# Performance work log

Hardware: AMD Instinct MI355X
Metric: run time of the kernel (lower is better)

Reference implementation:

```python
import jax, jax.numpy as jnp
import numpy as np

B, P, E = 64, 196, 2048      # batch, num_pixels (14*14), encoder_size
H, EMB, V = 512, 512, 10000  # hidden_size, embed_size, vocab_size
T_CAP = 50                   # hard-coded pred/alpha buffer length
T_MAX = T_CAP - 1            # max(decode_lengths) = max(lengths) - 1 = 49


def setup_inputs() -> dict:
    key = jax.random.key(0)
    ks = jax.random.split(key, 20)

    def lin(k, out_f, in_f):
        kw, kb = jax.random.split(k)
        s = 1.0 / np.sqrt(in_f)
        return (jax.random.uniform(kw, (out_f, in_f), jnp.float32, -s, s),
                jax.random.uniform(kb, (out_f,), jnp.float32, -s, s))

    features = jax.random.normal(ks[0], (B, P, E), jnp.float32)
    captions = jax.random.randint(ks[1], (B, T_CAP), 0, V)
    # sorted descending, first length forced to 50 so max(decode_lengths)=49
    lengths = jnp.sort(jax.random.randint(ks[2], (B,), 2, T_CAP + 1))[::-1]
    lengths = lengths.at[0].set(T_CAP)

    Wx_w, Wx_b = lin(ks[3], E, E)          # attention Wx: encoder->encoder
    Wh_w, Wh_b = lin(ks[4], E, H)          # attention Wh: hidden->encoder
    V_w, V_b = lin(ks[5], 1, E)            # attention V: encoder->1
    init_h_w, init_h_b = lin(ks[6], H, E)  # init_h
    f_beta_w, f_beta_b = lin(ks[7], E, H)  # f_beta gate
    embed_w = jax.random.normal(ks[8], (V, EMB), jnp.float32)
    gru_w_ih, gru_b_ih = lin(ks[9], 3 * H, E + EMB)
    gru_w_hh, gru_b_hh = lin(ks[10], 3 * H, H)
    fc1_w, fc1_b = lin(ks[11], V, H)

    return dict(features=features, captions=captions, lengths=lengths,
                Wx_w=Wx_w, Wx_b=Wx_b, Wh_w=Wh_w, Wh_b=Wh_b, V_w=V_w, V_b=V_b,
                init_h_w=init_h_w, init_h_b=init_h_b,
                f_beta_w=f_beta_w, f_beta_b=f_beta_b, embed_w=embed_w,
                gru_w_ih=gru_w_ih, gru_b_ih=gru_b_ih,
                gru_w_hh=gru_w_hh, gru_b_hh=gru_b_hh,
                fc1_w=fc1_w, fc1_b=fc1_b)


def reference(features, captions, lengths, Wx_w, Wx_b, Wh_w, Wh_b, V_w, V_b,
              init_h_w, init_h_b, f_beta_w, f_beta_b, embed_w,
              gru_w_ih, gru_b_ih, gru_w_hh, gru_b_hh, fc1_w, fc1_b):
    b, p, e = features.shape
    vsz = fc1_w.shape[0]
    dec = lengths - 1                                  # decode_lengths
    # init hidden state from mean-pooled features
    h0 = jnp.mean(features, axis=1) @ init_h_w.T + init_h_b      # [B,H]
    # Wx(features) is time-invariant: precompute once
    x_wx = jnp.einsum('bpe,fe->bpf', features, Wx_w) + Wx_b      # [B,P,E]
    emb = embed_w[captions]                                      # [B,50,EMB]
    emb_t = jnp.transpose(emb[:, :T_MAX], (1, 0, 2))             # [T,B,EMB]

    def step(h, xs):
        t, e_t = xs
        active = (dec >= t)                            # rows still decoding
        # Bahdanau attention
        h_wh = h @ Wh_w.T + Wh_b                       # [B,E]
        lam = jnp.einsum('bpe,oe->bpo',
                         jnp.tanh(x_wx + h_wh[:, None, :]), V_w) + V_b
        alpha = jax.nn.softmax(lam, axis=1)            # [B,P,1]
        z = jnp.sum(alpha * features, axis=1)          # [B,E]
        # sigmoid gate
        gate = jax.nn.sigmoid(h @ f_beta_w.T + f_beta_b)
        inp = jnp.concatenate([gate * z, e_t], axis=1)  # [B,E+EMB]
        # GRUCell (torch gate order r,z,n)
        gi = inp @ gru_w_ih.T + gru_b_ih
        gh = h @ gru_w_hh.T + gru_b_hh
        i_r, i_z, i_n = jnp.split(gi, 3, axis=-1)
        h_r, h_z, h_n = jnp.split(gh, 3, axis=-1)
        r = jax.nn.sigmoid(i_r + h_r)
        zg = jax.nn.sigmoid(i_z + h_z)
        n = jnp.tanh(i_n + r * h_n)
        h_new = (1.0 - zg) * n + zg * h
        pred = h_new @ fc1_w.T + fc1_b                 # dropout in eval = id
        m = active[:, None]
        h_out = jnp.where(m, h_new, h)                 # freeze finished rows
        return h_out, (jnp.where(m, pred, 0.0),
                       jnp.where(m, alpha[..., 0], 0.0))

    _, (preds_t, alphas_t) = jax.lax.scan(
        step, h0, (jnp.arange(T_MAX), emb_t))
    preds = jnp.zeros((b, T_CAP, vsz), features.dtype)
    preds = preds.at[:, :T_MAX].set(jnp.transpose(preds_t, (1, 0, 2)))
    alphas = jnp.zeros((b, T_CAP, p), features.dtype)
    alphas = alphas.at[:, :T_MAX].set(jnp.transpose(alphas_t, (1, 0, 2)))
    return preds, alphas, dec
```

## Files before the change

### kernel.cpp

```cpp
#include <hip/hip_runtime.h>
#include <cstddef>

#define B_    64
#define P_    196
#define E_    2048
#define H_    512
#define EMB_  512
#define V_    10000
#define TCAP_ 50
#define TMAX_ 49
#define KI_   2560
#define G3_   1536

typedef __attribute__((ext_vector_type(8))) short short8;
typedef __attribute__((ext_vector_type(4))) float floatx4;
typedef unsigned int u32;
typedef const __attribute__((address_space(1))) u32* gptr_t;
typedef __attribute__((address_space(3))) u32* lptr_t;

__device__ __forceinline__ unsigned short f2bf_rne(float f) {
    unsigned int x = __float_as_uint(f);
    unsigned int r = (x + 0x7fffu + ((x >> 16) & 1u)) >> 16;
    return (unsigned short)r;
}
__device__ __forceinline__ float bf2f(unsigned int u16) {
    return __uint_as_float(u16 << 16);
}
__device__ __forceinline__ float fast_tanh(float x) {
    float a = fabsf(x);
    float e = __expf(2.0f * a);
    float r = 1.0f - 2.0f / (e + 1.0f);
    return (x < 0.0f) ? -r : r;
}
__device__ __forceinline__ float fast_sig(float x) {
    return 1.0f / (1.0f + __expf(-x));
}

__global__ void init_out_kernel(float* __restrict__ preds, float* __restrict__ alphas,
                                float* __restrict__ dec, const int* __restrict__ lens)
{
    int i = blockIdx.x * 256 + threadIdx.x;
    if (i < B_ * V_) {
        int b = i / V_, v = i - b * V_;
        preds[((size_t)b * TCAP_ + TMAX_) * V_ + v] = 0.f;
    }
    if (i < B_ * P_) {
        int b = i / P_, p = i - b * P_;
        alphas[((size_t)b * TCAP_ + TMAX_) * P_ + p] = 0.f;
    }
    if (i < B_) dec[i] = (float)(lens[i] - 1);
}

__global__ void f2bf_kernel(const float* __restrict__ src, unsigned short* __restrict__ dst, int n8)
{
    int i = blockIdx.x * 256 + threadIdx.x;
    if (i >= n8) return;
    float4 a = ((const float4*)src)[2 * i];
    float4 b = ((const float4*)src)[2 * i + 1];
    uint4 o;
    o.x = (unsigned)f2bf_rne(a.x) | ((unsigned)f2bf_rne(a.y) << 16);
    o.y = (unsigned)f2bf_rne(a.z) | ((unsigned)f2bf_rne(a.w) << 16);
    o.z = (unsigned)f2bf_rne(b.x) | ((unsigned)f2bf_rne(b.y) << 16);
    o.w = (unsigned)f2bf_rne(b.z) | ((unsigned)f2bf_rne(b.w) << 16);
    ((uint4*)dst)[i] = o;
}

__global__ void mean_kernel(const float* __restrict__ f, unsigned short* __restrict__ out)
{
    int i = blockIdx.x * 256 + threadIdx.x;
    int b = i >> 11, e = i & 2047;
    const float* p = f + (size_t)b * P_ * E_ + e;
    float s = 0.f;
    #pragma unroll 4
    for (int k = 0; k < P_; ++k) s += p[(size_t)k * E_];
    out[i] = f2bf_rne(s * (1.0f / (float)P_));
}

__global__ void __launch_bounds__(256)
mfma_xwx_kernel(const unsigned short* __restrict__ A,
                const unsigned short* __restrict__ W,
                const float* __restrict__ bias,
                unsigned short* __restrict__ C)
{
    __shared__ unsigned short As[128 * 64];
    __shared__ unsigned short Bs[128 * 64];
    int wv = threadIdx.x >> 6, lane = threadIdx.x & 63;
    int mr = lane & 15, quad = lane >> 4;
    int m0 = blockIdx.y * 128;
    int n0 = blockIdx.x * 128;
    int wm = (wv & 1) * 64, wn = (wv >> 1) * 64;
    int srow = wv * 32;
    int lrow = lane >> 3;
    int lcol = (lane & 7) * 8;
    floatx4 acc[4][4] = {};
    for (int k0 = 0; k0 < E_; k0 += 64) {
        __syncthreads();
        #pragma unroll
        for (int i = 0; i < 4; ++i) {
            int r = srow + i * 8;
            __builtin_amdgcn_global_load_lds(
                (gptr_t)(A + (size_t)(m0 + r + lrow) * E_ + k0 + lcol),
                (lptr_t)(As + r * 64), 16, 0, 0);
            __builtin_amdgcn_global_load_lds(
                (gptr_t)(W + (size_t)(n0 + r + lrow) * E_ + k0 + lcol),
                (lptr_t)(Bs + r * 64), 16, 0, 0);
        }
        __syncthreads();
        #pragma unroll
        for (int kk = 0; kk < 64; kk += 32) {
            short8 af[4], bf[4];
            #pragma unroll
            for (int i = 0; i < 4; ++i)
                af[i] = *(const short8*)(As + (wm + i * 16 + mr) * 64 + kk + quad * 8);
            #pragma unroll
            for (int j = 0; j < 4; ++j)
                bf[j] = *(const short8*)(Bs + (wn + j * 16 + mr) * 64 + kk + quad * 8);
            #pragma unroll
            for (int i = 0; i < 4; ++i)
                #pragma unroll
                for (int j = 0; j < 4; ++j)
                    acc[i][j] = __builtin_amdgcn_mfma_f32_16x16x32_bf16(af[i], bf[j], acc[i][j], 0, 0, 0);
        }
    }
    #pragma unroll
    for (int j = 0; j < 4; ++j) {
        int col = n0 + wn + j * 16 + mr;
        float bs = bias[col];
        #pragma unroll
        for (int i = 0; i < 4; ++i) {
            int row = m0 + wm + i * 16 + quad * 4;
            #pragma unroll
            for (int ii = 0; ii < 4; ++ii)
                C[(size_t)(row + ii) * E_ + col] = f2bf_rne(acc[i][j][ii] + bs);
        }
    }
}

__global__ void __launch_bounds__(256)
fc1tile_kernel(const unsigned short* __restrict__ Hall,
               const unsigned short* __restrict__ W,
               const float* __restrict__ bias,
               float* __restrict__ preds, const int* __restrict__ lens)
{
    __shared__ unsigned short As[128 * 64];
    __shared__ unsigned short Bs[128 * 64];
    int wv = threadIdx.x >> 6, lane = threadIdx.x & 63;
    int mr = lane & 15, quad = lane >> 4;
    int m0 = blockIdx.y * 128;
    int n0 = blockIdx.x * 128;
    int wm = (wv & 1) * 64, wn = (wv >> 1) * 64;
    int srow = wv * 32;
    int lrow = lane >> 3;
    int lcol = (lane & 7) * 8;
    floatx4 acc[4][4] = {};
    for (int k0 = 0; k0 < H_; k0 += 64) {
        __syncthreads();
        #pragma unroll
        for (int i = 0; i < 4; ++i) {
            int r = srow + i * 8;
            __builtin_amdgcn_global_load_lds(
                (gptr_t)(Hall + (size_t)(m0 + r + lrow) * H_ + k0 + lcol),
                (lptr_t)(As + r * 64), 16, 0, 0);
            __builtin_amdgcn_global_load_lds(
                (gptr_t)(W + (size_t)(n0 + r + lrow) * H_ + k0 + lcol),
                (lptr_t)(Bs + r * 64), 16, 0, 0);
        }
        __syncthreads();
        #pragma unroll
        for (int kk = 0; kk < 64; kk += 32) {
            short8 af[4], bf[4];
            #pragma unroll
            for (int i = 0; i < 4; ++i)
                af[i] = *(const short8*)(As + (wm + i * 16 + mr) * 64 + kk + quad * 8);
            #pragma unroll
            for (int j = 0; j < 4; ++j)
                bf[j] = *(const short8*)(Bs + (wn + j * 16 + mr) * 64 + kk + quad * 8);
            #pragma unroll
            for (int i = 0; i < 4; ++i)
                #pragma unroll
                for (int j = 0; j < 4; ++j)
                    acc[i][j] = __builtin_amdgcn_mfma_f32_16x16x32_bf16(af[i], bf[j], acc[i][j], 0, 0, 0);
        }
    }
    #pragma unroll
    for (int j = 0; j < 4; ++j) {
        int col = n0 + wn + j * 16 + mr;
        float bs = bias[min(col, V_ - 1)];
        #pragma unroll
        for (int i = 0; i < 4; ++i) {
            int row = m0 + wm + i * 16 + quad * 4;
            #pragma unroll
            for (int ii = 0; ii < 4; ++ii) {
                int r = row + ii;
                if (r < TMAX_ * B_ && col < V_) {
                    int t = r >> 6, b = r & 63;
                    float v = (lens[b] > t) ? (acc[i][j][ii] + bs) : 0.f;
                    preds[((size_t)b * TCAP_ + t) * V_ + col] = v;
                }
            }
        }
    }
}

template<int KC>
__global__ void __launch_bounds__(256)
mfma_gemm64(const unsigned short* __restrict__ A, int ld,
            const unsigned short* __restrict__ W,
            const float* __restrict__ bias,
            float* __restrict__ C, unsigned short* __restrict__ Cbf, int ldc)
{
    int wv = threadIdx.x >> 6, lane = threadIdx.x & 63;
    int mr = lane & 15, quad = lane >> 4;
    int m0 = wv * 16;
    int n0 = blockIdx.x * 16;
    const unsigned short* pa = A + (size_t)(m0 + mr) * ld + quad * 8;
    const unsigned short* pb = W + (size_t)(n0 + mr) * ld + quad * 8;
    floatx4 acc = {0.f, 0.f, 0.f, 0.f};
    #pragma unroll 16
    for (int k0 = 0; k0 < KC; k0 += 32) {
        short8 a = *(const short8*)(const void*)(pa + k0);
        short8 b = *(const short8*)(const void*)(pb + k0);
        acc = __builtin_amdgcn_mfma_f32_16x16x32_bf16(a, b, acc, 0, 0, 0);
    }
    int col = n0 + mr;
    float bs = bias ? bias[col] : 0.f;
    #pragma unroll
    for (int i = 0; i < 4; ++i) {
        int row = m0 + quad * 4 + i;
        float v = acc[i] + bs;
        C[(size_t)row * ldc + col] = v;
        if (Cbf) Cbf[(size_t)row * ldc + col] = f2bf_rne(v);
    }
}

__global__ void __launch_bounds__(256)
mfma_h3(const unsigned short* __restrict__ hbf,
        const unsigned short* __restrict__ whbf, const float* __restrict__ Wh_b,
        const unsigned short* __restrict__ fbbf, const float* __restrict__ fb_b,
        const unsigned short* __restrict__ ghhbf, const float* __restrict__ ghh_b,
        float* __restrict__ hwh, float* __restrict__ hf, float* __restrict__ gh)
{
    int bt = blockIdx.x;
    const unsigned short* W; const float* bias; float* C; int n0; int ldc;
    if (bt < 128)      { W = whbf;  bias = Wh_b;  C = hwh; n0 = bt * 16;         ldc = E_; }
    else if (bt < 256) { W = fbbf;  bias = fb_b;  C = hf;  n0 = (bt - 128) * 16; ldc = E_; }
    else               { W = ghhbf; bias = ghh_b; C = gh;  n0 = (bt - 256) * 16; ldc = G3_; }
    int wv = threadIdx.x >> 6, lane = threadIdx.x & 63;
    int mr = lane & 15, quad = lane >> 4;
    int m0 = wv * 16;
    const unsigned short* pa = hbf + (size_t)(m0 + mr) * H_ + quad * 8;
    const unsigned short* pb = W + (size_t)(n0 + mr) * H_ + quad * 8;
    floatx4 acc0 = {0.f, 0.f, 0.f, 0.f};
    floatx4 acc1 = {0.f, 0.f, 0.f, 0.f};
    #pragma unroll
    for (int k0 = 0; k0 < 256; k0 += 32) {
        short8 a0 = *(const short8*)(const void*)(pa + k0);
        short8 b0 = *(const short8*)(const void*)(pb + k0);
        acc0 = __builtin_amdgcn_mfma_f32_16x16x32_bf16(a0, b0, acc0, 0, 0, 0);
        short8 a1 = *(const short8*)(const void*)(pa + k0 + 256);
        short8 b1 = *(const short8*)(const void*)(pb + k0 + 256);
        acc1 = __builtin_amdgcn_mfma_f32_16x16x32_bf16(a1, b1, acc1, 0, 0, 0);
    }
    floatx4 acc = acc0 + acc1;
    int col = n0 + mr;
    float bs = bias[col];
    #pragma unroll
    for (int i = 0; i < 4; ++i) {
        int row = m0 + quad * 4 + i;
        C[(size_t)row * ldc + col] = acc[i] + bs;
    }
}

__global__ void __launch_bounds__(256)
lam_kernel(const unsigned short* __restrict__ xwx, const float* __restrict__ hwh,
           const float* __restrict__ Vw, const float* __restrict__ Vb,
           float* __restrict__ lam)
{
    __shared__ float sh[E_];
    __shared__ float sv[E_];
    int b = blockIdx.y;
    int p0 = blockIdx.x * 16;
    int tid = threadIdx.x;
    {
        const float4* hs = (const float4*)(hwh + (size_t)b * E_);
        const float4* vs = (const float4*)Vw;
        ((float4*)sh)[tid]       = hs[tid];
        ((float4*)sh)[tid + 256] = hs[tid + 256];
        ((float4*)sv)[tid]       = vs[tid];
        ((float4*)sv)[tid + 256] = vs[tid + 256];
    }
    __syncthreads();
    int wv = tid >> 6, lane = tid & 63;
    #pragma unroll
    for (int r = 0; r < 4; ++r) {
        int p = p0 + wv * 4 + r;
        if (p < P_) {
            const unsigned short* px = xwx + ((size_t)b * P_ + p) * E_;
            float acc = 0.f;
            #pragma unroll
            for (int it = 0; it < 4; ++it) {
                int e = it * 512 + lane * 8;
                uint4 u = *(const uint4*)(const void*)(px + e);
                float4 h0 = *(const float4*)(sh + e);
                float4 h1 = *(const float4*)(sh + e + 4);
                float4 v0 = *(const float4*)(sv + e);
                float4 v1 = *(const float4*)(sv + e + 4);
                acc = fmaf(fast_tanh(bf2f(u.x & 0xffffu) + h0.x), v0.x, acc);
                acc = fmaf(fast_tanh(bf2f(u.x >> 16)     + h0.y), v0.y, acc);
                acc = fmaf(fast_tanh(bf2f(u.y & 0xffffu) + h0.z), v0.z, acc);
                acc = fmaf(fast_tanh(bf2f(u.y >> 16)     + h0.w), v0.w, acc);
                acc = fmaf(fast_tanh(bf2f(u.z & 0xffffu) + h1.x), v1.x, acc);
                acc = fmaf(fast_tanh(bf2f(u.z >> 16)     + h1.y), v1.y, acc);
                acc = fmaf(fast_tanh(bf2f(u.w & 0xffffu) + h1.z), v1.z, acc);
                acc = fmaf(fast_tanh(bf2f(u.w >> 16)     + h1.w), v1.w, acc);
            }
            #pragma unroll
            for (int off = 32; off > 0; off >>= 1) acc += __shfl_down(acc, off);
            if (lane == 0) lam[b * P_ + p] = acc + Vb[0];
        }
    }
}

__global__ void __launch_bounds__(256)
attn_z_kernel(const unsigned short* __restrict__ fbf, const float* __restrict__ lam,
              const float* __restrict__ hf, const float* __restrict__ embed_w,
              const int* __restrict__ captions, const int* __restrict__ lens,
              unsigned short* __restrict__ inpbf, float* __restrict__ alphas, int t)
{
    int b = blockIdx.y;
    int tile = blockIdx.x;
    int tid = threadIdx.x;
    if (tile == 4) {
        int cap = captions[b * TCAP_ + t];
        const float* e = embed_w + (size_t)cap * EMB_;
        int c = tid * 2;
        float2 v = *(const float2*)(e + c);
        *(unsigned int*)(inpbf + (size_t)b * KI_ + E_ + c) =
            (unsigned)f2bf_rne(v.x) | ((unsigned)f2bf_rne(v.y) << 16);
        return;
    }
    __shared__ float sa[256];
    __shared__ float sr[256];
    __shared__ float psum[4][64][8];
    float x = (tid < P_) ? lam[b * P_ + tid] : -1e30f;
    sr[tid] = x;
    __syncthreads();
    for (int s = 128; s > 0; s >>= 1) {
        if (tid < s) sr[tid] = fmaxf(sr[tid], sr[tid + s]);
        __syncthreads();
    }
    float mx = sr[0];
    __syncthreads();
    float ex = (tid < P_) ? __expf(x - mx) : 0.f;
    sa[tid] = ex;
    sr[tid] = ex;
    __syncthreads();
    for (int s = 128; s > 0; s >>= 1) {
        if (tid < s) sr[tid] += sr[tid + s];
        __syncthreads();
    }
    float inv = 1.0f / sr[0];
    if (tile == 0 && tid < P_) {
        alphas[(size_t)b * TCAP_ * P_ + (size_t)t * P_ + tid] = (lens[b] > t) ? ex * inv : 0.f;
    }
    int wv = tid >> 6, lane = tid & 63;
    int e0 = tile * 512;
    const unsigned short* fp = fbf + ((size_t)b * P_ + wv * 49) * E_ + e0 + lane * 8;
    float acc[8] = {0.f,0.f,0.f,0.f,0.f,0.f,0.f,0.f};
    #pragma unroll 7
    for (int i = 0; i < 49; ++i) {
        uint4 u = *(const uint4*)(const void*)(fp + (size_t)i * E_);
        float ap = sa[wv * 49 + i];
        acc[0] = fmaf(ap, bf2f(u.x & 0xffffu), acc[0]);
        acc[1] = fmaf(ap, bf2f(u.x >> 16),     acc[1]);
        acc[2] = fmaf(ap, bf2f(u.y & 0xffffu), acc[2]);
        acc[3] = fmaf(ap, bf2f(u.y >> 16),     acc[3]);
        acc[4] = fmaf(ap, bf2f(u.z & 0xffffu), acc[4]);
        acc[5] = fmaf(ap, bf2f(u.z >> 16),     acc[5]);
        acc[6] = fmaf(ap, bf2f(u.w & 0xffffu), acc[6]);
        acc[7] = fmaf(ap, bf2f(u.w >> 16),     acc[7]);
    }
    #pragma unroll
    for (int k = 0; k < 8; ++k) psum[wv][lane][k] = acc[k];
    __syncthreads();
    int c0 = tid * 2;
    int lc = c0 >> 3, kc = c0 & 7;
    float2 s = {0.f, 0.f};
    #pragma unroll
    for (int w2 = 0; w2 < 4; ++w2) {
        float2 v = *(const float2*)&psum[w2][lc][kc];
        s.x += v.x; s.y += v.y;
    }
    s.x *= inv; s.y *= inv;
    float2 gv = *(const float2*)(hf + (size_t)b * E_ + e0 + c0);
    float g0 = fast_sig(gv.x), g1 = fast_sig(gv.y);
    *(unsigned int*)(inpbf + (size_t)b * KI_ + e0 + c0) =
        (unsigned)f2bf_rne(g0 * s.x) | ((unsigned)f2bf_rne(g1 * s.y) << 16);
}

__global__ void __launch_bounds__(256)
gigru_kernel(const unsigned short* __restrict__ inpbf,
             const unsigned short* __restrict__ wihbf,
             const float* __restrict__ b_ih,
             const float* __restrict__ gh,
             const int* __restrict__ lens,
             float* __restrict__ h, unsigned short* __restrict__ hbf,
             unsigned short* __restrict__ Hall, int t)
{
    __shared__ float red[4][3][16][17];
    int wv = threadIdx.x >> 6, lane = threadIdx.x & 63;
    int mr = lane & 15, quad = lane >> 4;
    int j0 = blockIdx.x * 16;
    int m0 = blockIdx.y * 16;
    int koff = wv * 640;
    const unsigned short* pa = inpbf + (size_t)(m0 + mr) * KI_ + koff + quad * 8;
    const unsigned short* pb0 = wihbf + (size_t)(j0 + mr) * KI_ + koff + quad * 8;
    const unsigned short* pb1 = pb0 + (size_t)512 * KI_;
    const unsigned short* pb2 = pb0 + (size_t)1024 * KI_;
    floatx4 ar = {0.f,0.f,0.f,0.f}, az = {0.f,0.f,0.f,0.f}, an = {0.f,0.f,0.f,0.f};
    #pragma unroll 4
    for (int k0 = 0; k0 < 640; k0 += 32) {
        short8 a = *(const short8*)(const void*)(pa + k0);
        short8 br = *(const short8*)(const void*)(pb0 + k0);
        short8 bz = *(const short8*)(const void*)(pb1 + k0);
        short8 bn = *(const short8*)(const void*)(pb2 + k0);
        ar = __builtin_amdgcn_mfma_f32_16x16x32_bf16(a, br, ar, 0, 0, 0);
        az = __builtin_amdgcn_mfma_f32_16x16x32_bf16(a, bz, az, 0, 0, 0);
        an = __builtin_amdgcn_mfma_f32_16x16x32_bf16(a, bn, an, 0, 0, 0);
    }
    #pragma unroll
    for (int i = 0; i < 4; ++i) {
        red[wv][0][quad * 4 + i][mr] = ar[i];
        red[wv][1][quad * 4 + i][mr] = az[i];
        red[wv][2][quad * 4 + i][mr] = an[i];
    }
    __syncthreads();
    int row = threadIdx.x >> 4, col = threadIdx.x & 15;
    int b = m0 + row, j = j0 + col;
    float ir = red[0][0][row][col] + red[1][0][row][col] + red[2][0][row][col] + red[3][0][row][col] + b_ih[j];
    float iz = red[0][1][row][col] + red[1][1][row][col] + red[2][1][row][col] + red[3][1][row][col] + b_ih[512 + j];
    float in_= red[0][2][row][col] + red[1][2][row][col] + red[2][2][row][col] + red[3][2][row][col] + b_ih[1024 + j];
    float hr = gh[(size_t)b * G3_ + j];
    float hz = gh[(size_t)b * G3_ + 512 + j];
    float hn = gh[(size_t)b * G3_ + 1024 + j];
    float r  = fast_sig(ir + hr);
    float zg = fast_sig(iz + hz);
    float n  = fast_tanh(in_ + r * hn);
    float hp = h[(size_t)b * H_ + j];
    float hv = (1.f - zg) * n + zg * hp;
    float ho = (lens[b] > t) ? hv : hp;
    h[(size_t)b * H_ + j] = ho;
    unsigned short hob = f2bf_rne(ho);
    hbf[(size_t)b * H_ + j] = hob;
    Hall[((size_t)t * B_ + b) * H_ + j] = hob;
}

extern "C" void kernel_launch(void* const* d_in, const int* in_sizes, int n_in,
                              void* d_out, int out_size, void* d_ws, size_t ws_size,
                              hipStream_t stream)
{
    const float* features  = (const float*)d_in[0];
    const int*   captions  = (const int*)d_in[1];
    const int*   lengths   = (const int*)d_in[2];
    const float* Wx_w      = (const float*)d_in[3];
    const float* Wx_b      = (const float*)d_in[4];
    const float* Wh_w      = (const float*)d_in[5];
    const float* Wh_b      = (const float*)d_in[6];
    const float* V_w       = (const float*)d_in[7];
    const float* V_b       = (const float*)d_in[8];
    const float* init_h_w  = (const float*)d_in[9];
    const float* init_h_b  = (const float*)d_in[10];
    const float* f_beta_w  = (const float*)d_in[11];
    const float* f_beta_b  = (const float*)d_in[12];
    const float* embed_w   = (const float*)d_in[13];
    const float* gru_w_ih  = (const float*)d_in[14];
    const float* gru_b_ih  = (const float*)d_in[15];
    const float* gru_w_hh  = (const float*)d_in[16];
    const float* gru_b_hh  = (const float*)d_in[17];
    const float* fc1_w     = (const float*)d_in[18];
    const float* fc1_b     = (const float*)d_in[19];

    float* preds  = (float*)d_out;
    float* alphas = preds + (size_t)B_ * TCAP_ * V_;
    float* dec    = alphas + (size_t)B_ * TCAP_ * P_;

    char* w = (char*)d_ws;
    unsigned short* fbf     = (unsigned short*)w; w += (size_t)12544 * 2048 * 2;
    unsigned short* xwx     = (unsigned short*)w; w += (size_t)12544 * 2048 * 2;
    unsigned short* wxbf    = (unsigned short*)w; w += (size_t)2048 * 2048 * 2;
    unsigned short* whbf    = (unsigned short*)w; w += (size_t)2048 * 512 * 2;
    unsigned short* fbbf    = (unsigned short*)w; w += (size_t)2048 * 512 * 2;
    unsigned short* ghhbf   = (unsigned short*)w; w += (size_t)1536 * 512 * 2;
    unsigned short* wihbf   = (unsigned short*)w; w += (size_t)1536 * 2560 * 2;
    unsigned short* fc1bf   = (unsigned short*)w; w += (size_t)10112 * 512 * 2;
    unsigned short* ihwbf   = (unsigned short*)w; w += (size_t)512 * 2048 * 2;
    unsigned short* fmeanbf = (unsigned short*)w; w += (size_t)64 * 2048 * 2;
    unsigned short* hbf     = (unsigned short*)w; w += (size_t)64 * 512 * 2;
    unsigned short* inpbf   = (unsigned short*)w; w += (size_t)64 * KI_ * 2;
    unsigned short* Hall    = (unsigned short*)w; w += (size_t)3200 * 512 * 2;
    float* h   = (float*)w; w += (size_t)64 * 512 * 4;
    float* hwh = (float*)w; w += (size_t)64 * 2048 * 4;
    float* hf  = (float*)w; w += (size_t)64 * 2048 * 4;
    float* gh  = (float*)w; w += (size_t)64 * 1536 * 4;
    float* lam = (float*)w; w += (size_t)64 * 196 * 4;

    init_out_kernel<<<2500, 256, 0, stream>>>(preds, alphas, dec, lengths);

    f2bf_kernel<<<12544, 256, 0, stream>>>(features, fbf, 12544 * 2048 / 8);
    f2bf_kernel<<<2048, 256, 0, stream>>>(Wx_w, wxbf, 2048 * 2048 / 8);
    f2bf_kernel<<<512, 256, 0, stream>>>(Wh_w, whbf, 2048 * 512 / 8);
    f2bf_kernel<<<512, 256, 0, stream>>>(f_beta_w, fbbf, 2048 * 512 / 8);
    f2bf_kernel<<<384, 256, 0, stream>>>(gru_w_hh, ghhbf, 1536 * 512 / 8);
    f2bf_kernel<<<1920, 256, 0, stream>>>(gru_w_ih, wihbf, 1536 * 2560 / 8);
    f2bf_kernel<<<2500, 256, 0, stream>>>(fc1_w, fc1bf, 10000 * 512 / 8);
    f2bf_kernel<<<512, 256, 0, stream>>>(init_h_w, ihwbf, 512 * 2048 / 8);

    mean_kernel<<<512, 256, 0, stream>>>(features, fmeanbf);
    mfma_gemm64<2048><<<32, 256, 0, stream>>>(fmeanbf, 2048, ihwbf, init_h_b, h, hbf, 512);
    mfma_xwx_kernel<<<dim3(16, 98), 256, 0, stream>>>(fbf, wxbf, Wx_b, xwx);

    for (int t = 0; t < TMAX_; ++t) {
        mfma_h3<<<352, 256, 0, stream>>>(hbf, whbf, Wh_b, fbbf, f_beta_b, ghhbf, gru_b_hh,
                                         hwh, hf, gh);
        lam_kernel<<<dim3(13, 64), 256, 0, stream>>>(xwx, hwh, V_w, V_b, lam);
        attn_z_kernel<<<dim3(5, 64), 256, 0, stream>>>(fbf, lam, hf, embed_w, captions,
                                                       lengths, inpbf, alphas, t);
        gigru_kernel<<<dim3(32, 4), 256, 0, stream>>>(inpbf, wihbf, gru_b_ih, gh,
                                                      lengths, h, hbf, Hall, t);
    }
    fc1tile_kernel<<<dim3(79, 25), 256, 0, stream>>>(Hall, fc1bf, fc1_b, preds, lengths);
}
```

Before: 3.326 ms.

## Fuse recurrent decode loop into persistent kernel with atomic grid barriers

Replaces the 49x4 per-timestep kernel launches with one persistent 512-block kernel that runs every decode step, separating the phases with an atomic-counter grid barrier. The attention-context phase is also re-split from 5 tiles per batch to 8 column chunks of 256, and softmax reductions now use wave shuffles. This is meant to remove launch overhead and inter-kernel gaps on a latency-bound recurrence. The cost is that it depends on all 512 blocks being co-resident (256 CUs at 2 blocks each), and the spin barrier adds atomic traffic; the barrier also uses no cooperative launch, so a deadlock is possible if occupancy assumptions fail.

```diff
diff --git a/kernel.cpp b/kernel.cpp
--- a/kernel.cpp
+++ b/kernel.cpp
@@ -11,6 +11,7 @@
 #define TMAX_ 49
 #define KI_   2560
 #define G3_   1536
+#define NBLK_ 512
 
 typedef __attribute__((ext_vector_type(8))) short short8;
 typedef __attribute__((ext_vector_type(4))) float floatx4;
@@ -36,10 +37,25 @@
     return 1.0f / (1.0f + __expf(-x));
 }
 
+__device__ __forceinline__ void gbar(unsigned int* cnt, unsigned int target)
+{
+    __syncthreads();
+    if (threadIdx.x == 0) {
+        __threadfence();
+        atomicAdd(cnt, 1u);
+        while (__hip_atomic_load(cnt, __ATOMIC_RELAXED, __HIP_MEMORY_SCOPE_AGENT) < target)
+            __builtin_amdgcn_s_sleep(2);
+        __threadfence();
+    }
+    __syncthreads();
+}
+
 __global__ void init_out_kernel(float* __restrict__ preds, float* __restrict__ alphas,
-                                float* __restrict__ dec, const int* __restrict__ lens)
+                                float* __restrict__ dec, const int* __restrict__ lens,
+                                unsigned int* __restrict__ barcnt)
 {
     int i = blockIdx.x * 256 + threadIdx.x;
+    if (i == 0) *barcnt = 0u;
     if (i < B_ * V_) {
         int b = i / V_, v = i - b * V_;
         preds[((size_t)b * TCAP_ + TMAX_) * V_ + v] = 0.f;
@@ -233,226 +249,205 @@
     }
 }
 
-__global__ void __launch_bounds__(256)
-mfma_h3(const unsigned short* __restrict__ hbf,
-        const unsigned short* __restrict__ whbf, const float* __restrict__ Wh_b,
-        const unsigned short* __restrict__ fbbf, const float* __restrict__ fb_b,
-        const unsigned short* __restrict__ ghhbf, const float* __restrict__ ghh_b,
-        float* __restrict__ hwh, float* __restrict__ hf, float* __restrict__ gh)
-{
-    int bt = blockIdx.x;
-    const unsigned short* W; const float* bias; float* C; int n0; int ldc;
-    if (bt < 128)      { W = whbf;  bias = Wh_b;  C = hwh; n0 = bt * 16;         ldc = E_; }
-    else if (bt < 256) { W = fbbf;  bias = fb_b;  C = hf;  n0 = (bt - 128) * 16; ldc = E_; }
-    else               { W = ghhbf; bias = ghh_b; C = gh;  n0 = (bt - 256) * 16; ldc = G3_; }
-    int wv = threadIdx.x >> 6, lane = threadIdx.x & 63;
-    int mr = lane & 15, quad = lane >> 4;
-    int m0 = wv * 16;
-    const unsigned short* pa = hbf + (size_t)(m0 + mr) * H_ + quad * 8;
-    const unsigned short* pb = W + (size_t)(n0 + mr) * H_ + quad * 8;
-    floatx4 acc0 = {0.f, 0.f, 0.f, 0.f};
-    floatx4 acc1 = {0.f, 0.f, 0.f, 0.f};
-    #pragma unroll
-    for (int k0 = 0; k0 < 256; k0 += 32) {
-        short8 a0 = *(const short8*)(const void*)(pa + k0);
-        short8 b0 = *(const short8*)(const void*)(pb + k0);
-        acc0 = __builtin_amdgcn_mfma_f32_16x16x32_bf16(a0, b0, acc0, 0, 0, 0);
-        short8 a1 = *(const short8*)(const void*)(pa + k0 + 256);
-        short8 b1 = *(const short8*)(const void*)(pb + k0 + 256);
-        acc1 = __builtin_amdgcn_mfma_f32_16x16x32_bf16(a1, b1, acc1, 0, 0, 0);
-    }
-    floatx4 acc = acc0 + acc1;
-    int col = n0 + mr;
-    float bs = bias[col];
-    #pragma unroll
-    for (int i = 0; i < 4; ++i) {
-        int row = m0 + quad * 4 + i;
-        C[(size_t)row * ldc + col] = acc[i] + bs;
-    }
-}
-
-__global__ void __launch_bounds__(256)
-lam_kernel(const unsigned short* __restrict__ xwx, const float* __restrict__ hwh,
-           const float* __restrict__ Vw, const float* __restrict__ Vb,
-           float* __restrict__ lam)
-{
-    __shared__ float sh[E_];
-    __shared__ float sv[E_];
-    int b = blockIdx.y;
-    int p0 = blockIdx.x * 16;
-    int tid = threadIdx.x;
-    {
-        const float4* hs = (const float4*)(hwh + (size_t)b * E_);
-        const float4* vs = (const float4*)Vw;
-        ((float4*)sh)[tid]       = hs[tid];
-        ((float4*)sh)[tid + 256] = hs[tid + 256];
-        ((float4*)sv)[tid]       = vs[tid];
-        ((float4*)sv)[tid + 256] = vs[tid + 256];
-    }
-    __syncthreads();
-    int wv = tid >> 6, lane = tid & 63;
-    #pragma unroll
-    for (int r = 0; r < 4; ++r) {
-        int p = p0 + wv * 4 + r;
-        if (p < P_) {
-            const unsigned short* px = xwx + ((size_t)b * P_ + p) * E_;
-            float acc = 0.f;
-            #pragma unroll
-            for (int it = 0; it < 4; ++it) {
-                int e = it * 512 + lane * 8;
-                uint4 u = *(const uint4*)(const void*)(px + e);
-                float4 h0 = *(const float4*)(sh + e);
-                float4 h1 = *(const float4*)(sh + e + 4);
-                float4 v0 = *(const float4*)(sv + e);
-                float4 v1 = *(const float4*)(sv + e + 4);
-                acc = fmaf(fast_tanh(bf2f(u.x & 0xffffu) + h0.x), v0.x, acc);
-                acc = fmaf(fast_tanh(bf2f(u.x >> 16)     + h0.y), v0.y, acc);
-                acc = fmaf(fast_tanh(bf2f(u.y & 0xffffu) + h0.z), v0.z, acc);
-                acc = fmaf(fast_tanh(bf2f(u.y >> 16)     + h0.w), v0.w, acc);
-                acc = fmaf(fast_tanh(bf2f(u.z & 0xffffu) + h1.x), v1.x, acc);
-                acc = fmaf(fast_tanh(bf2f(u.z >> 16)     + h1.y), v1.y, acc);
-                acc = fmaf(fast_tanh(bf2f(u.w & 0xffffu) + h1.z), v1.z, acc);
-                acc = fmaf(fast_tanh(bf2f(u.w >> 16)     + h1.w), v1.w, acc);
-            }
-            #pragma unroll
-            for (int off = 32; off > 0; off >>= 1) acc += __shfl_down(acc, off);
-            if (lane == 0) lam[b * P_ + p] = acc + Vb[0];
-        }
-    }
-}
-
-__global__ void __launch_bounds__(256)
-attn_z_kernel(const unsigned short* __restrict__ fbf, const float* __restrict__ lam,
-              const float* __restrict__ hf, const float* __restrict__ embed_w,
-              const int* __restrict__ captions, const int* __restrict__ lens,
-              unsigned short* __restrict__ inpbf, float* __restrict__ alphas, int t)
-{
-    int b = blockIdx.y;
-    int tile = blockIdx.x;
-    int tid = threadIdx.x;
-    if (tile == 4) {
-        int cap = captions[b * TCAP_ + t];
-        const float* e = embed_w + (size_t)cap * EMB_;
-        int c = tid * 2;
-        float2 v = *(const float2*)(e + c);
-        *(unsigned int*)(inpbf + (size_t)b * KI_ + E_ + c) =
-            (unsigned)f2bf_rne(v.x) | ((unsigned)f2bf_rne(v.y) << 16);
-        return;
-    }
-    __shared__ float sa[256];
-    __shared__ float sr[256];
-    __shared__ float psum[4][64][8];
-    float x = (tid < P_) ? lam[b * P_ + tid] : -1e30f;
-    sr[tid] = x;
-    __syncthreads();
-    for (int s = 128; s > 0; s >>= 1) {
-        if (tid < s) sr[tid] = fmaxf(sr[tid], sr[tid + s]);
-        __syncthreads();
-    }
-    float mx = sr[0];
-    __syncthreads();
-    float ex = (tid < P_) ? __expf(x - mx) : 0.f;
-    sa[tid] = ex;
-    sr[tid] = ex;
-    __syncthreads();
-    for (int s = 128; s > 0; s >>= 1) {
-        if (tid < s) sr[tid] += sr[tid + s];
-        __syncthreads();
-    }
-    float inv = 1.0f / sr[0];
-    if (tile == 0 && tid < P_) {
-        alphas[(size_t)b * TCAP_ * P_ + (size_t)t * P_ + tid] = (lens[b] > t) ? ex * inv : 0.f;
-    }
-    int wv = tid >> 6, lane = tid & 63;
-    int e0 = tile * 512;
-    const unsigned short* fp = fbf + ((size_t)b * P_ + wv * 49) * E_ + e0 + lane * 8;
-    float acc[8] = {0.f,0.f,0.f,0.f,0.f,0.f,0.f,0.f};
-    #pragma unroll 7
-    for (int i = 0; i < 49; ++i) {
-        uint4 u = *(const uint4*)(const void*)(fp + (size_t)i * E_);
-        float ap = sa[wv * 49 + i];
-        acc[0] = fmaf(ap, bf2f(u.x & 0xffffu), acc[0]);
-        acc[1] = fmaf(ap, bf2f(u.x >> 16),     acc[1]);
-        acc[2] = fmaf(ap, bf2f(u.y & 0xffffu), acc[2]);
-        acc[3] = fmaf(ap, bf2f(u.y >> 16),     acc[3]);
-        acc[4] = fmaf(ap, bf2f(u.z & 0xffffu), acc[4]);
-        acc[5] = fmaf(ap, bf2f(u.z >> 16),     acc[5]);
-        acc[6] = fmaf(ap, bf2f(u.w & 0xffffu), acc[6]);
-        acc[7] = fmaf(ap, bf2f(u.w >> 16),     acc[7]);
-    }
-    #pragma unroll
-    for (int k = 0; k < 8; ++k) psum[wv][lane][k] = acc[k];
-    __syncthreads();
-    int c0 = tid * 2;
-    int lc = c0 >> 3, kc = c0 & 7;
-    float2 s = {0.f, 0.f};
-    #pragma unroll
-    for (int w2 = 0; w2 < 4; ++w2) {
-        float2 v = *(const float2*)&psum[w2][lc][kc];
-        s.x += v.x; s.y += v.y;
-    }
-    s.x *= inv; s.y *= inv;
-    float2 gv = *(const float2*)(hf + (size_t)b * E_ + e0 + c0);
-    float g0 = fast_sig(gv.x), g1 = fast_sig(gv.y);
-    *(unsigned int*)(inpbf + (size_t)b * KI_ + e0 + c0) =
-        (unsigned)f2bf_rne(g0 * s.x) | ((unsigned)f2bf_rne(g1 * s.y) << 16);
-}
-
-__global__ void __launch_bounds__(256)
-gigru_kernel(const unsigned short* __restrict__ inpbf,
-             const unsigned short* __restrict__ wihbf,
-             const float* __restrict__ b_ih,
-             const float* __restrict__ gh,
-             const int* __restrict__ lens,
-             float* __restrict__ h, unsigned short* __restrict__ hbf,
-             unsigned short* __restrict__ Hall, int t)
-{
-    __shared__ float red[4][3][16][17];
-    int wv = threadIdx.x >> 6, lane = threadIdx.x & 63;
-    int mr = lane & 15, quad = lane >> 4;
-    int j0 = blockIdx.x * 16;
-    int m0 = blockIdx.y * 16;
-    int koff = wv * 640;
-    const unsigned short* pa = inpbf + (size_t)(m0 + mr) * KI_ + koff + quad * 8;
-    const unsigned short* pb0 = wihbf + (size_t)(j0 + mr) * KI_ + koff + quad * 8;
-    const unsigned short* pb1 = pb0 + (size_t)512 * KI_;
-    const unsigned short* pb2 = pb0 + (size_t)1024 * KI_;
-    floatx4 ar = {0.f,0.f,0.f,0.f}, az = {0.f,0.f,0.f,0.f}, an = {0.f,0.f,0.f,0.f};
-    #pragma unroll 4
-    for (int k0 = 0; k0 < 640; k0 += 32) {
-        short8 a = *(const short8*)(const void*)(pa + k0);
-        short8 br = *(const short8*)(const void*)(pb0 + k0);
-        short8 bz = *(const short8*)(const void*)(pb1 + k0);
-        short8 bn = *(const short8*)(const void*)(pb2 + k0);
-        ar = __builtin_amdgcn_mfma_f32_16x16x32_bf16(a, br, ar, 0, 0, 0);
-        az = __builtin_amdgcn_mfma_f32_16x16x32_bf16(a, bz, az, 0, 0, 0);
-        an = __builtin_amdgcn_mfma_f32_16x16x32_bf16(a, bn, an, 0, 0, 0);
-    }
-    #pragma unroll
-    for (int i = 0; i < 4; ++i) {
-        red[wv][0][quad * 4 + i][mr] = ar[i];
-        red[wv][1][quad * 4 + i][mr] = az[i];
-        red[wv][2][quad * 4 + i][mr] = an[i];
-    }
-    __syncthreads();
-    int row = threadIdx.x >> 4, col = threadIdx.x & 15;
-    int b = m0 + row, j = j0 + col;
-    float ir = red[0][0][row][col] + red[1][0][row][col] + red[2][0][row][col] + red[3][0][row][col] + b_ih[j];
-    float iz = red[0][1][row][col] + red[1][1][row][col] + red[2][1][row][col] + red[3][1][row][col] + b_ih[512 + j];
-    float in_= red[0][2][row][col] + red[1][2][row][col] + red[2][2][row][col] + red[3][2][row][col] + b_ih[1024 + j];
-    float hr = gh[(size_t)b * G3_ + j];
-    float hz = gh[(size_t)b * G3_ + 512 + j];
-    float hn = gh[(size_t)b * G3_ + 1024 + j];
-    float r  = fast_sig(ir + hr);
-    float zg = fast_sig(iz + hz);
-    float n  = fast_tanh(in_ + r * hn);
-    float hp = h[(size_t)b * H_ + j];
-    float hv = (1.f - zg) * n + zg * hp;
-    float ho = (lens[b] > t) ? hv : hp;
-    h[(size_t)b * H_ + j] = ho;
-    unsigned short hob = f2bf_rne(ho);
-    hbf[(size_t)b * H_ + j] = hob;
-    Hall[((size_t)t * B_ + b) * H_ + j] = hob;
+__global__ void __launch_bounds__(256, 2)
+loop_kernel(unsigned short* __restrict__ hbf,
+            const unsigned short* __restrict__ whbf, const float* __restrict__ Wh_b,
+            const unsigned short* __restrict__ fbbf, const float* __restrict__ fb_b,
+            const unsigned short* __restrict__ ghhbf, const float* __restrict__ ghh_b,
+            float* __restrict__ hwh, float* __restrict__ hf, float* __restrict__ gh,
+            const unsigned short* __restrict__ xwx,
+            const float* __restrict__ Vw, const float* __restrict__ Vb,
+            float* __restrict__ lam,
+            const unsigned short* __restrict__ fbf,
+            const float* __restrict__ embed_w,
+            const int* __restrict__ captions, const int* __restrict__ lens,
+            unsigned short* __restrict__ inpbf,
+            float* __restrict__ alphas,
+            const unsigned short* __restrict__ wihbf, const float* __restrict__ b_ih,
+            float* __restrict__ h, unsigned short* __restrict__ Hall,
+            unsigned int* __restrict__ barcnt)
+{
+    __shared__ float smem[4096];
+    const int bid = blockIdx.x;
+    const int tid = threadIdx.x;
+    const int wv = tid >> 6, lane = tid & 63;
+    const int mr = lane & 15, quad = lane >> 4;
+    unsigned int ep = 0;
+
+    for (int t = 0; t < TMAX_; ++t) {
+        if (bid < 352) {
+            const unsigned short* W; const float* bias; float* C; int n0; int ldc;
+            if (bid < 128)      { W = whbf;  bias = Wh_b;  C = hwh; n0 = bid * 16;         ldc = E_; }
+            else if (bid < 256) { W = fbbf;  bias = fb_b;  C = hf;  n0 = (bid - 128) * 16; ldc = E_; }
+            else                { W = ghhbf; bias = ghh_b; C = gh;  n0 = (bid - 256) * 16; ldc = G3_; }
+            int m0 = wv * 16;
+            const unsigned short* pa = hbf + (size_t)(m0 + mr) * H_ + quad * 8;
+            const unsigned short* pb = W + (size_t)(n0 + mr) * H_ + quad * 8;
+            floatx4 acc0 = {0.f, 0.f, 0.f, 0.f};
+            floatx4 acc1 = {0.f, 0.f, 0.f, 0.f};
+            #pragma unroll
+            for (int k0 = 0; k0 < 256; k0 += 32) {
+                short8 a0 = *(const short8*)(const void*)(pa + k0);
+                short8 b0 = *(const short8*)(const void*)(pb + k0);
+                acc0 = __builtin_amdgcn_mfma_f32_16x16x32_bf16(a0, b0, acc0, 0, 0, 0);
+                short8 a1 = *(const short8*)(const void*)(pa + k0 + 256);
+                short8 b1 = *(const short8*)(const void*)(pb + k0 + 256);
+                acc1 = __builtin_amdgcn_mfma_f32_16x16x32_bf16(a1, b1, acc1, 0, 0, 0);
+            }
+            floatx4 acc = acc0 + acc1;
+            int col = n0 + mr;
+            float bs = bias[col];
+            #pragma unroll
+            for (int i = 0; i < 4; ++i)
+                C[(size_t)(m0 + quad * 4 + i) * ldc + col] = acc[i] + bs;
+        }
+        gbar(barcnt, (++ep) * (unsigned)NBLK_);
+
+        {
+            int b = bid >> 3, q = bid & 7;
+            float* sh = smem;
+            float* sv = smem + 2048;
+            const float4* hs = (const float4*)(hwh + (size_t)b * E_);
+            const float4* vs = (const float4*)Vw;
+            ((float4*)sh)[tid]       = hs[tid];
+            ((float4*)sh)[tid + 256] = hs[tid + 256];
+            ((float4*)sv)[tid]       = vs[tid];
+            ((float4*)sv)[tid + 256] = vs[tid + 256];
+            __syncthreads();
+            float vb0 = Vb[0];
+            #pragma unroll
+            for (int i = 0; i < 7; ++i) {
+                int pl = wv + i * 4;
+                int p = q * 25 + pl;
+                if (pl < 25 && p < P_) {
+                    const unsigned short* px = xwx + ((size_t)b * P_ + p) * E_;
+                    float acc = 0.f;
+                    #pragma unroll
+                    for (int it = 0; it < 4; ++it) {
+                        int e = it * 512 + lane * 8;
+                        uint4 u = *(const uint4*)(const void*)(px + e);
+                        float4 h0 = *(const float4*)(sh + e);
+                        float4 h1 = *(const float4*)(sh + e + 4);
+                        float4 v0 = *(const float4*)(sv + e);
+                        float4 v1 = *(const float4*)(sv + e + 4);
+                        acc = fmaf(fast_tanh(bf2f(u.x & 0xffffu) + h0.x), v0.x, acc);
+                        acc = fmaf(fast_tanh(bf2f(u.x >> 16)     + h0.y), v0.y, acc);
+                        acc = fmaf(fast_tanh(bf2f(u.y & 0xffffu) + h0.z), v0.z, acc);
+                        acc = fmaf(fast_tanh(bf2f(u.y >> 16)     + h0.w), v0.w, acc);
+                        acc = fmaf(fast_tanh(bf2f(u.z & 0xffffu) + h1.x), v1.x, acc);
+                        acc = fmaf(fast_tanh(bf2f(u.z >> 16)     + h1.y), v1.y, acc);
+                        acc = fmaf(fast_tanh(bf2f(u.w & 0xffffu) + h1.z), v1.z, acc);
+                        acc = fmaf(fast_tanh(bf2f(u.w >> 16)     + h1.w), v1.w, acc);
+                    }
+                    #pragma unroll
+                    for (int off = 32; off > 0; off >>= 1) acc += __shfl_down(acc, off);
+                    if (lane == 0) lam[b * P_ + p] = acc + vb0;
+                }
+            }
+        }
+        gbar(barcnt, (++ep) * (unsigned)NBLK_);
+
+        {
+            int b = bid >> 3, c = bid & 7;
+            int e0 = c * 256;
+            float* sa = smem;
+            float* sr = smem + 256;
+            float* ps = smem + 512;
+            float x = (tid < P_) ? lam[b * P_ + tid] : -1e30f;
+            float mxl = x;
+            #pragma unroll
+            for (int off = 32; off > 0; off >>= 1) mxl = fmaxf(mxl, __shfl_xor(mxl, off));
+            if (lane == 0) sr[wv] = mxl;
+            __syncthreads();
+            float mx = fmaxf(fmaxf(sr[0], sr[1]), fmaxf(sr[2], sr[3]));
+            float ex = (tid < P_) ? __expf(x - mx) : 0.f;
+            sa[tid] = ex;
+            float sml = ex;
+            #pragma unroll
+            for (int off = 32; off > 0; off >>= 1) sml += __shfl_xor(sml, off);
+            if (lane == 0) sr[4 + wv] = sml;
+            __syncthreads();
+            float inv = 1.f / (sr[4] + sr[5] + sr[6] + sr[7]);
+            if (c == 0 && tid < P_)
+                alphas[(size_t)b * TCAP_ * P_ + (size_t)t * P_ + tid] = (lens[b] > t) ? ex * inv : 0.f;
+            if (c == 1) {
+                int cap = captions[b * TCAP_ + t];
+                float2 v = *(const float2*)(embed_w + (size_t)cap * EMB_ + tid * 2);
+                *(u32*)(inpbf + (size_t)b * KI_ + E_ + tid * 2) =
+                    (u32)f2bf_rne(v.x) | ((u32)f2bf_rne(v.y) << 16);
+            }
+            int half = tid >> 7, li = tid & 127;
+            const unsigned short* fp = fbf + ((size_t)b * P_ + half) * E_ + e0 + li * 2;
+            float a0 = 0.f, a1 = 0.f;
+            #pragma unroll 7
+            for (int p = half; p < P_; p += 2) {
+                u32 u = *(const u32*)(const void*)fp;
+                fp += 2 * E_;
+                float wgt = sa[p];
+                a0 = fmaf(wgt, bf2f(u & 0xffffu), a0);
+                a1 = fmaf(wgt, bf2f(u >> 16), a1);
+            }
+            ps[tid * 2]     = a0;
+            ps[tid * 2 + 1] = a1;
+            __syncthreads();
+            if (tid < 128) {
+                float z0 = (ps[tid * 2]     + ps[(tid + 128) * 2])     * inv;
+                float z1 = (ps[tid * 2 + 1] + ps[(tid + 128) * 2 + 1]) * inv;
+                float2 gv = *(const float2*)(hf + (size_t)b * E_ + e0 + tid * 2);
+                *(u32*)(inpbf + (size_t)b * KI_ + e0 + tid * 2) =
+                    (u32)f2bf_rne(fast_sig(gv.x) * z0) | ((u32)f2bf_rne(fast_sig(gv.y) * z1) << 16);
+            }
+        }
+        gbar(barcnt, (++ep) * (unsigned)NBLK_);
+
+        if (bid < 128) {
+            float (*red)[3][16][17] = (float (*)[3][16][17])smem;
+            int j0 = (bid & 31) * 16;
+            int m0 = (bid >> 5) * 16;
+            int koff = wv * 640;
+            const unsigned short* pa  = inpbf + (size_t)(m0 + mr) * KI_ + koff + quad * 8;
+            const unsigned short* pb0 = wihbf + (size_t)(j0 + mr) * KI_ + koff + quad * 8;
+            const unsigned short* pb1 = pb0 + (size_t)512 * KI_;
+            const unsigned short* pb2 = pb0 + (size_t)1024 * KI_;
+            floatx4 ar = {0.f,0.f,0.f,0.f}, az = {0.f,0.f,0.f,0.f}, an = {0.f,0.f,0.f,0.f};
+            #pragma unroll 4
+            for (int k0 = 0; k0 < 640; k0 += 32) {
+                short8 a  = *(const short8*)(const void*)(pa + k0);
+                short8 br = *(const short8*)(const void*)(pb0 + k0);
+                short8 bz = *(const short8*)(const void*)(pb1 + k0);
+                short8 bn = *(const short8*)(const void*)(pb2 + k0);
+                ar = __builtin_amdgcn_mfma_f32_16x16x32_bf16(a, br, ar, 0, 0, 0);
+                az = __builtin_amdgcn_mfma_f32_16x16x32_bf16(a, bz, az, 0, 0, 0);
+                an = __builtin_amdgcn_mfma_f32_16x16x32_bf16(a, bn, an, 0, 0, 0);
+            }
+            #pragma unroll
+            for (int i = 0; i < 4; ++i) {
+                red[wv][0][quad * 4 + i][mr] = ar[i];
+                red[wv][1][quad * 4 + i][mr] = az[i];
+                red[wv][2][quad * 4 + i][mr] = an[i];
+            }
+            __syncthreads();
+            int row = tid >> 4, col = tid & 15;
+            int b = m0 + row, j = j0 + col;
+            float ir = red[0][0][row][col] + red[1][0][row][col] + red[2][0][row][col] + red[3][0][row][col] + b_ih[j];
+            float iz = red[0][1][row][col] + red[1][1][row][col] + red[2][1][row][col] + red[3][1][row][col] + b_ih[512 + j];
+            float in_= red[0][2][row][col] + red[1][2][row][col] + red[2][2][row][col] + red[3][2][row][col] + b_ih[1024 + j];
+            float hr = gh[(size_t)b * G3_ + j];
+            float hz = gh[(size_t)b * G3_ + 512 + j];
+            float hn = gh[(size_t)b * G3_ + 1024 + j];
+            float r  = fast_sig(ir + hr);
+            float zg = fast_sig(iz + hz);
+            float n  = fast_tanh(in_ + r * hn);
+            float hp = h[(size_t)b * H_ + j];
+            float hv = (1.f - zg) * n + zg * hp;
+            float ho = (lens[b] > t) ? hv : hp;
+            h[(size_t)b * H_ + j] = ho;
+            unsigned short hob = f2bf_rne(ho);
+            hbf[(size_t)b * H_ + j] = hob;
+            Hall[((size_t)t * B_ + b) * H_ + j] = hob;
+        }
+        gbar(barcnt, (++ep) * (unsigned)NBLK_);
+    }
 }
 
 extern "C" void kernel_launch(void* const* d_in, const int* in_sizes, int n_in,
@@ -503,8 +498,9 @@
     float* hf  = (float*)w; w += (size_t)64 * 2048 * 4;
     float* gh  = (float*)w; w += (size_t)64 * 1536 * 4;
     float* lam = (float*)w; w += (size_t)64 * 196 * 4;
-
-    init_out_kernel<<<2500, 256, 0, stream>>>(preds, alphas, dec, lengths);
+    unsigned int* barcnt = (unsigned int*)w; w += 256;
+
+    init_out_kernel<<<2500, 256, 0, stream>>>(preds, alphas, dec, lengths, barcnt);
 
     f2bf_kernel<<<12544, 256, 0, stream>>>(features, fbf, 12544 * 2048 / 8);
     f2bf_kernel<<<2048, 256, 0, stream>>>(Wx_w, wxbf, 2048 * 2048 / 8);
@@ -519,14 +515,10 @@
     mfma_gemm64<2048><<<32, 256, 0, stream>>>(fmeanbf, 2048, ihwbf, init_h_b, h, hbf, 512);
     mfma_xwx_kernel<<<dim3(16, 98), 256, 0, stream>>>(fbf, wxbf, Wx_b, xwx);
 
-    for (int t = 0; t < TMAX_; ++t) {
-        mfma_h3<<<352, 256, 0, stream>>>(hbf, whbf, Wh_b, fbbf, f_beta_b, ghhbf, gru_b_hh,
-                                         hwh, hf, gh);
-        lam_kernel<<<dim3(13, 64), 256, 0, stream>>>(xwx, hwh, V_w, V_b, lam);
-        attn_z_kernel<<<dim3(5, 64), 256, 0, stream>>>(fbf, lam, hf, embed_w, captions,
-                                                       lengths, inpbf, alphas, t);
-        gigru_kernel<<<dim3(32, 4), 256, 0, stream>>>(inpbf, wihbf, gru_b_ih, gh,
-                                                      lengths, h, hbf, Hall, t);
-    }
+    loop_kernel<<<NBLK_, 256, 0, stream>>>(hbf, whbf, Wh_b, fbbf, f_beta_b, ghhbf, gru_b_hh,
+                                           hwh, hf, gh, xwx, V_w, V_b, lam, fbf, embed_w,
+                                           captions, lengths, inpbf, alphas, wihbf, gru_b_ih,
+                                           h, Hall, barcnt);
+
     fc1tile_kernel<<<dim3(79, 25), 256, 0, stream>>>(Hall, fc1bf, fc1_b, preds, lengths);
 }
```

After: 12.92 ms. +288.6%, slower.
